# Optimization experiments

Hardware: AMD Instinct MI355X
Metric: run time of the kernel (lower is better)

The kernel has to match this reference:

```python
import jax, jax.numpy as jnp
import numpy as np

INPUT_DIM = 1024
HEAD_DIM = 64
BATCH = 4
SEQ = 2048


def setup_inputs() -> dict:
    key = jax.random.key(0)
    ks = jax.random.split(key, 7)
    scale = 1.0 / np.sqrt(INPUT_DIM)
    x = jax.random.normal(ks[0], (BATCH, SEQ, INPUT_DIM), dtype=jnp.float32)
    Wq = jax.random.uniform(ks[1], (INPUT_DIM, HEAD_DIM), jnp.float32, -scale, scale)
    bq = jax.random.uniform(ks[2], (HEAD_DIM,), jnp.float32, -scale, scale)
    Wk = jax.random.uniform(ks[3], (INPUT_DIM, HEAD_DIM), jnp.float32, -scale, scale)
    bk = jax.random.uniform(ks[4], (HEAD_DIM,), jnp.float32, -scale, scale)
    Wv = jax.random.uniform(ks[5], (INPUT_DIM, HEAD_DIM), jnp.float32, -scale, scale)
    bv = jax.random.uniform(ks[6], (HEAD_DIM,), jnp.float32, -scale, scale)
    return {"x": x, "Wq": Wq, "bq": bq, "Wk": Wk, "bk": bk, "Wv": Wv, "bv": bv}


def reference(x, Wq, bq, Wk, bk, Wv, bv):
    # q,k,v: [B, S, Hd]
    q = jnp.einsum('bsd,dh->bsh', x, Wq) + bq
    k = jnp.einsum('bsd,dh->bsh', x, Wk) + bk
    v = jnp.einsum('bsd,dh->bsh', x, Wv) + bv
    scores = jnp.einsum('bqh,bkh->bqk', q, k)  # [B, S, S]
    S = scores.shape[-1]
    # causal mask: 0 on/below diagonal, -inf above (matches torch triu().T trick)
    causal = jnp.tril(jnp.ones((S, S), dtype=bool))
    scores = jnp.where(causal, scores, -jnp.inf)
    # original divides by sqrt(head_dim) AFTER adding mask (-inf stays -inf)
    scores = scores / jnp.sqrt(jnp.asarray(q.shape[-1], scores.dtype))
    attn = jax.nn.softmax(scores, axis=-1)
    return jnp.einsum('bqk,bkh->bqh', attn, v)
```

## Files before the change

### kernel.cpp

```cpp
#include <hip/hip_runtime.h>

#define SEQ  2048
#define DIM  1024
#define HD   64
#define AW   4

typedef float f32x4  __attribute__((ext_vector_type(4)));
typedef short bf16x8 __attribute__((ext_vector_type(8)));

__device__ __forceinline__ short f2bf(float x) {
    union { float f; unsigned u; } v; v.f = x;
    unsigned r = v.u + 0x7FFFu + ((v.u >> 16) & 1u);
    return (short)(r >> 16);
}
__device__ __forceinline__ short f2bf_fast(float x) {
    union { float f; unsigned u; } v; v.f = x;
    return (short)((v.u + 0x8000u) >> 16);
}

#define MFMA16(a, b, c) __builtin_amdgcn_mfma_f32_16x16x32_bf16((a), (b), (c), 0, 0, 0)

__global__ __launch_bounds__(256) void wprep_kernel(
    const float* __restrict__ Wq, const float* __restrict__ Wk,
    const float* __restrict__ Wv, short* __restrict__ wfrag)
{
    const int idx = blockIdx.x * 256 + threadIdx.x;
    const int l  = idx & 63;
    const int n  = (idx >> 6) & 3;
    const int ks = (idx >> 8) & 31;
    const int w  = idx >> 13;
    const float* __restrict__ W = (w == 0) ? Wq : (w == 1) ? Wk : Wv;
    bf16x8 v;
#pragma unroll
    for (int j = 0; j < 8; ++j)
        v[j] = f2bf(W[(size_t)(ks * 32 + (l >> 4) * 8 + j) * HD + n * 16 + (l & 15)]);
    *reinterpret_cast<bf16x8*>(wfrag + (size_t)idx * 8) = v;
}

__global__ __launch_bounds__(256) void proj_kernel(
    const float* __restrict__ x, const short* __restrict__ wfrag,
    const float* __restrict__ bq, const float* __restrict__ bk,
    const float* __restrict__ bv,
    short* __restrict__ Qs, short* __restrict__ Kb, short* __restrict__ Vt)
{
    __shared__ __align__(16) char smem[49152 + 2304];

    const int tid  = threadIdx.x;
    const int lane = tid & 63;
    const int w    = tid >> 6;
    const int c    = lane & 15;
    const int g    = lane >> 4;
    const int r0   = blockIdx.x * 16;

    f32x4 acc[3][4] = {};
    for (int ks = w * 8; ks < w * 8 + 8; ++ks) {
        const float* xp = x + (size_t)(r0 + c) * DIM + ks * 32 + g * 8;
        float4 a0 = *reinterpret_cast<const float4*>(xp);
        float4 a1 = *reinterpret_cast<const float4*>(xp + 4);
        float av[8] = {a0.x, a0.y, a0.z, a0.w, a1.x, a1.y, a1.z, a1.w};
        bf16x8 af;
#pragma unroll
        for (int j = 0; j < 8; ++j) af[j] = f2bf_fast(av[j]);
#pragma unroll
        for (int which = 0; which < 3; ++which)
#pragma unroll
            for (int n = 0; n < 4; ++n) {
                bf16x8 bfr = *reinterpret_cast<const bf16x8*>(
                    wfrag + ((size_t)((which * 32 + ks) * 4 + n) * 64 + lane) * 8);
                acc[which][n] = MFMA16(af, bfr, acc[which][n]);
            }
    }

    f32x4* red = (f32x4*)smem;
#pragma unroll
    for (int which = 0; which < 3; ++which)
#pragma unroll
        for (int n = 0; n < 4; ++n)
            red[((which * 4 + n) * 4 + w) * 64 + lane] = acc[which][n];
    __syncthreads();

    if (w < 3) {
        const float* __restrict__ bias = (w == 0) ? bq : (w == 1) ? bk : bv;
        f32x4 sum[4];
#pragma unroll
        for (int n = 0; n < 4; ++n) {
            sum[n] = red[((w * 4 + n) * 4 + 0) * 64 + lane];
#pragma unroll
            for (int s = 1; s < 4; ++s)
                sum[n] += red[((w * 4 + n) * 4 + s) * 64 + lane];
        }
        if (w < 2) {
            short* __restrict__ o = (w == 0) ? Qs : Kb;
            const float sc = (w == 0) ? 0.125f : 1.0f;
#pragma unroll
            for (int n = 0; n < 4; ++n) {
                const float bb = bias[n * 16 + c];
#pragma unroll
                for (int i = 0; i < 4; ++i)
                    o[(size_t)(r0 + g * 4 + i) * HD + n * 16 + c] =
                        f2bf((sum[n][i] + bb) * sc);
            }
        } else {
            short* ts = (short*)(smem + 49152);
#pragma unroll
            for (int n = 0; n < 4; ++n) {
                const float bb = bias[n * 16 + c];
#pragma unroll
                for (int i = 0; i < 4; ++i)
                    ts[(g * 4 + i) * 72 + n * 16 + c] = f2bf(sum[n][i] + bb);
            }
            bf16x8 o0, o1;
#pragma unroll
            for (int e = 0; e < 8; ++e) o0[e] = ts[e * 72 + lane];
#pragma unroll
            for (int e = 0; e < 8; ++e) o1[e] = ts[(8 + e) * 72 + lane];
            const int b  = r0 >> 11;
            const int sb = r0 & (SEQ - 1);
            short* dst = Vt + (((size_t)(b * 64 + lane)) << 11) + sb;
            *reinterpret_cast<bf16x8*>(dst)     = o0;
            *reinterpret_cast<bf16x8*>(dst + 8) = o1;
        }
    }
}

__device__ __forceinline__ void loadK(
    const short* __restrict__ Kb, size_t krow0, int key0, int c, int g,
    bf16x8 (&kf)[4][2])
{
#pragma unroll
    for (int n = 0; n < 4; ++n)
#pragma unroll
        for (int st = 0; st < 2; ++st)
            kf[n][st] = *reinterpret_cast<const bf16x8*>(
                Kb + (krow0 + key0 + n * 16 + c) * HD + st * 32 + g * 8);
}

__device__ __forceinline__ void tile_step(
    const short* __restrict__ Vt, int batch, int t, int tlast, int qbase,
    int c, int g, short* P, bf16x8 qf0, bf16x8 qf1,
    const bf16x8 (&kf)[4][2],
    f32x4 (&O)[4], float (&m_i)[4], float (&l_i)[4])
{
    const int key0 = t * 64;

    bf16x8 vf[2][4];
#pragma unroll
    for (int st = 0; st < 2; ++st)
#pragma unroll
        for (int n = 0; n < 4; ++n)
            vf[st][n] = *reinterpret_cast<const bf16x8*>(
                Vt + (((size_t)(batch * 64 + n * 16 + c)) << 11) + key0 + st * 32 + g * 8);

    f32x4 S[4] = {};
#pragma unroll
    for (int n = 0; n < 4; ++n) {
        S[n] = MFMA16(qf0, kf[n][0], S[n]);
        S[n] = MFMA16(qf1, kf[n][1], S[n]);
    }
    if (t == tlast) {
#pragma unroll
        for (int n = 0; n < 4; ++n)
#pragma unroll
            for (int i = 0; i < 4; ++i)
                if (key0 + n * 16 + c > qbase + g * 4 + i)
                    S[n][i] = -__builtin_inff();
    }
    float mx[4], corr[4], rs[4];
#pragma unroll
    for (int i = 0; i < 4; ++i)
        mx[i] = fmaxf(fmaxf(S[0][i], S[1][i]), fmaxf(S[2][i], S[3][i]));
#pragma unroll
    for (int off = 1; off <= 8; off <<= 1)
#pragma unroll
        for (int i = 0; i < 4; ++i)
            mx[i] = fmaxf(mx[i], __shfl_xor(mx[i], off, 64));
#pragma unroll
    for (int i = 0; i < 4; ++i) {
        const float mn = fmaxf(m_i[i], mx[i]);
        corr[i] = __expf(m_i[i] - mn);
        m_i[i] = mn;
        rs[i] = 0.f;
    }
#pragma unroll
    for (int n = 0; n < 4; ++n)
#pragma unroll
        for (int i = 0; i < 4; ++i) {
            const float p = __expf(S[n][i] - m_i[i]);
            S[n][i] = p;
            rs[i] += p;
        }
#pragma unroll
    for (int off = 1; off <= 8; off <<= 1)
#pragma unroll
        for (int i = 0; i < 4; ++i)
            rs[i] += __shfl_xor(rs[i], off, 64);
#pragma unroll
    for (int i = 0; i < 4; ++i) l_i[i] = l_i[i] * corr[i] + rs[i];
#pragma unroll
    for (int n = 0; n < 4; ++n)
#pragma unroll
        for (int i = 0; i < 4; ++i) O[n][i] *= corr[i];
#pragma unroll
    for (int n = 0; n < 4; ++n)
#pragma unroll
        for (int i = 0; i < 4; ++i)
            P[(g * 4 + i) * 72 + n * 16 + c] = f2bf_fast(S[n][i]);
#pragma unroll
    for (int st = 0; st < 2; ++st) {
        bf16x8 pf = *reinterpret_cast<const bf16x8*>(&P[c * 72 + st * 32 + g * 8]);
#pragma unroll
        for (int n = 0; n < 4; ++n)
            O[n] = MFMA16(pf, vf[st][n], O[n]);
    }
}

__global__ __launch_bounds__(256) void attn_fused_kernel(
    const short* __restrict__ Qs, const short* __restrict__ Kb,
    const short* __restrict__ Vt, float* __restrict__ out)
{
    __shared__ float  Ost[AW][2][16][68];
    __shared__ float2 mlst[AW][2][16];
    __shared__ short  Pw[AW][16 * 72];

    const int tid  = threadIdx.x;
    const int lane = tid & 63;
    const int w    = tid >> 6;
    const int c    = lane & 15;
    const int g    = lane >> 4;

    const int batch = blockIdx.x >> 6;
    const int p     = blockIdx.x & 63;
    const int qlocA = p;
    const int qlocB = 127 - p;
    const int ntA   = (qlocA >> 2) + 1;
    const int ntB   = (qlocB >> 2) + 1;
    const int qbA   = batch * 128 + qlocA;
    const int qbB   = batch * 128 + qlocB;

    bf16x8 qfA0 = *reinterpret_cast<const bf16x8*>(Qs + (size_t)(qbA * 16 + c) * HD + g * 8);
    bf16x8 qfA1 = *reinterpret_cast<const bf16x8*>(Qs + (size_t)(qbA * 16 + c) * HD + 32 + g * 8);
    bf16x8 qfB0 = *reinterpret_cast<const bf16x8*>(Qs + (size_t)(qbB * 16 + c) * HD + g * 8);
    bf16x8 qfB1 = *reinterpret_cast<const bf16x8*>(Qs + (size_t)(qbB * 16 + c) * HD + 32 + g * 8);

    f32x4 OA[4] = {}, OB[4] = {};
    float mA[4], lA[4], mB[4], lB[4];
#pragma unroll
    for (int i = 0; i < 4; ++i) {
        mA[i] = -__builtin_inff(); lA[i] = 0.f;
        mB[i] = -__builtin_inff(); lB[i] = 0.f;
    }

    short* P = Pw[w];
    const size_t krow0 = (size_t)batch * SEQ;

    bf16x8 kf[4][2], kfn[4][2];
    if (w < 33) {
        const int t0 = (w < ntA) ? w : w - ntA;
        loadK(Kb, krow0, t0 * 64, c, g, kf);
    }
    for (int idx = w; idx < 33; idx += AW) {
        const int nidx = idx + AW;
        int tn;
        if (nidx < 33) tn = (nidx < ntA) ? nidx : nidx - ntA;
        else           tn = (idx  < ntA) ? idx  : idx  - ntA;
        loadK(Kb, krow0, tn * 64, c, g, kfn);

        if (idx < ntA)
            tile_step(Vt, batch, idx, ntA - 1, qlocA * 16,
                      c, g, P, qfA0, qfA1, kf, OA, mA, lA);
        else
            tile_step(Vt, batch, idx - ntA, ntB - 1, qlocB * 16,
                      c, g, P, qfB0, qfB1, kf, OB, mB, lB);

#pragma unroll
        for (int n = 0; n < 4; ++n) {
            kf[n][0] = kfn[n][0];
            kf[n][1] = kfn[n][1];
        }
    }

#pragma unroll
    for (int n = 0; n < 4; ++n)
#pragma unroll
        for (int i = 0; i < 4; ++i) {
            Ost[w][0][g * 4 + i][n * 16 + c] = OA[n][i];
            Ost[w][1][g * 4 + i][n * 16 + c] = OB[n][i];
        }
    if (c == 0) {
#pragma unroll
        for (int i = 0; i < 4; ++i) {
            mlst[w][0][g * 4 + i] = make_float2(mA[i], lA[i]);
            mlst[w][1][g * 4 + i] = make_float2(mB[i], lB[i]);
        }
    }
    __syncthreads();

    {
        const int s  = w >> 1;
        const int qb = (w >> 1) ? qbB : qbA;
#pragma unroll
        for (int ri = 0; ri < 8; ++ri) {
            const int row = (w & 1) * 8 + ri;
            float M = -__builtin_inff();
#pragma unroll
            for (int wv = 0; wv < AW; ++wv)
                M = fmaxf(M, mlst[wv][s][row].x);
            float l = 0.f, o = 0.f;
#pragma unroll
            for (int wv = 0; wv < AW; ++wv) {
                const float2 ml = mlst[wv][s][row];
                const float wgt = __expf(ml.x - M);
                l += wgt * ml.y;
                o += wgt * Ost[wv][s][row][lane];
            }
            out[(size_t)(qb * 16 + row) * HD + lane] = o / l;
        }
    }
}

extern "C" void kernel_launch(void* const* d_in, const int* in_sizes, int n_in,
                              void* d_out, int out_size, void* d_ws, size_t ws_size,
                              hipStream_t stream)
{
    (void)in_sizes; (void)n_in; (void)out_size; (void)ws_size;
    const float* x  = (const float*)d_in[0];
    const float* Wq = (const float*)d_in[1];
    const float* bq = (const float*)d_in[2];
    const float* Wk = (const float*)d_in[3];
    const float* bk = (const float*)d_in[4];
    const float* Wv = (const float*)d_in[5];
    const float* bv = (const float*)d_in[6];
    float* out = (float*)d_out;

    char* ws = (char*)d_ws;
    short* Qs    = (short*)(ws);
    short* Kb    = (short*)(ws + (1u << 20));
    short* Vt    = (short*)(ws + (2u << 20));
    short* wfrag = (short*)(ws + (3u << 20));

    wprep_kernel<<<96, 256, 0, stream>>>(Wq, Wk, Wv, wfrag);
    proj_kernel<<<512, 256, 0, stream>>>(x, wfrag, bq, bk, bv, Qs, Kb, Vt);
    attn_fused_kernel<<<256, 256, 0, stream>>>(Qs, Kb, Vt, out);
}
```

Measured before the change: 43.45 us.

## Share K/V tile loads across paired query blocks and use exp2 softmax

The attention loop is restructured so that for key tiles both paired query blocks need (t < ntA), each K and V tile is loaded once and used for both query blocks, with separate P buffers per block. The remaining tiles for the long query block run in a second loop that prefetches K. Softmax switches to exp2f, with log2(e) folded into the Q scale factor, so each exponential skips a multiply. The shared-tile loop drops the K register prefetch, which may expose more load latency, and it raises register pressure because two S accumulators are live at once.

```diff
diff --git a/kernel.cpp b/kernel.cpp
--- a/kernel.cpp
+++ b/kernel.cpp
@@ -19,6 +19,8 @@
 }
 
 #define MFMA16(a, b, c) __builtin_amdgcn_mfma_f32_16x16x32_bf16((a), (b), (c), 0, 0, 0)
+
+#define QSCALE 0.18033688011f
 
 __global__ __launch_bounds__(256) void wprep_kernel(
     const float* __restrict__ Wq, const float* __restrict__ Wk,
@@ -91,7 +93,7 @@
         }
         if (w < 2) {
             short* __restrict__ o = (w == 0) ? Qs : Kb;
-            const float sc = (w == 0) ? 0.125f : 1.0f;
+            const float sc = (w == 0) ? QSCALE : 1.0f;
 #pragma unroll
             for (int n = 0; n < 4; ++n) {
                 const float bb = bias[n * 16 + c];
@@ -134,30 +136,34 @@
             kf[n][st] = *reinterpret_cast<const bf16x8*>(
                 Kb + (krow0 + key0 + n * 16 + c) * HD + st * 32 + g * 8);
 }
-
-__device__ __forceinline__ void tile_step(
-    const short* __restrict__ Vt, int batch, int t, int tlast, int qbase,
-    int c, int g, short* P, bf16x8 qf0, bf16x8 qf1,
-    const bf16x8 (&kf)[4][2],
-    f32x4 (&O)[4], float (&m_i)[4], float (&l_i)[4])
-{
-    const int key0 = t * 64;
-
-    bf16x8 vf[2][4];
+__device__ __forceinline__ void loadV(
+    const short* __restrict__ Vt, int batch, int key0, int c, int g,
+    bf16x8 (&vf)[2][4])
+{
 #pragma unroll
     for (int st = 0; st < 2; ++st)
 #pragma unroll
         for (int n = 0; n < 4; ++n)
             vf[st][n] = *reinterpret_cast<const bf16x8*>(
                 Vt + (((size_t)(batch * 64 + n * 16 + c)) << 11) + key0 + st * 32 + g * 8);
-
-    f32x4 S[4] = {};
+}
+
+__device__ __forceinline__ void qk16(
+    const bf16x8 (&kf)[4][2], bf16x8 q0, bf16x8 q1, f32x4 (&S)[4])
+{
 #pragma unroll
     for (int n = 0; n < 4; ++n) {
-        S[n] = MFMA16(qf0, kf[n][0], S[n]);
-        S[n] = MFMA16(qf1, kf[n][1], S[n]);
-    }
-    if (t == tlast) {
+        S[n] = MFMA16(q0, kf[n][0], S[n]);
+        S[n] = MFMA16(q1, kf[n][1], S[n]);
+    }
+}
+
+__device__ __forceinline__ void smax_pv(
+    f32x4 (&S)[4], bool diag, int key0, int qbase, int c, int g,
+    short* P, const bf16x8 (&vf)[2][4],
+    f32x4 (&O)[4], float (&m_i)[4], float (&l_i)[4])
+{
+    if (diag) {
 #pragma unroll
         for (int n = 0; n < 4; ++n)
 #pragma unroll
@@ -177,7 +183,7 @@
 #pragma unroll
     for (int i = 0; i < 4; ++i) {
         const float mn = fmaxf(m_i[i], mx[i]);
-        corr[i] = __expf(m_i[i] - mn);
+        corr[i] = exp2f(m_i[i] - mn);
         m_i[i] = mn;
         rs[i] = 0.f;
     }
@@ -185,7 +191,7 @@
     for (int n = 0; n < 4; ++n)
 #pragma unroll
         for (int i = 0; i < 4; ++i) {
-            const float p = __expf(S[n][i] - m_i[i]);
+            const float p = exp2f(S[n][i] - m_i[i]);
             S[n][i] = p;
             rs[i] += p;
         }
@@ -220,7 +226,7 @@
 {
     __shared__ float  Ost[AW][2][16][68];
     __shared__ float2 mlst[AW][2][16];
-    __shared__ short  Pw[AW][16 * 72];
+    __shared__ short  Pw[AW][2][16 * 72];
 
     const int tid  = threadIdx.x;
     const int lane = tid & 63;
@@ -250,32 +256,39 @@
         mB[i] = -__builtin_inff(); lB[i] = 0.f;
     }
 
-    short* P = Pw[w];
+    short* PA = Pw[w][0];
+    short* PB = Pw[w][1];
     const size_t krow0 = (size_t)batch * SEQ;
 
-    bf16x8 kf[4][2], kfn[4][2];
-    if (w < 33) {
-        const int t0 = (w < ntA) ? w : w - ntA;
-        loadK(Kb, krow0, t0 * 64, c, g, kf);
-    }
-    for (int idx = w; idx < 33; idx += AW) {
-        const int nidx = idx + AW;
-        int tn;
-        if (nidx < 33) tn = (nidx < ntA) ? nidx : nidx - ntA;
-        else           tn = (idx  < ntA) ? idx  : idx  - ntA;
-        loadK(Kb, krow0, tn * 64, c, g, kfn);
-
-        if (idx < ntA)
-            tile_step(Vt, batch, idx, ntA - 1, qlocA * 16,
-                      c, g, P, qfA0, qfA1, kf, OA, mA, lA);
-        else
-            tile_step(Vt, batch, idx - ntA, ntB - 1, qlocB * 16,
-                      c, g, P, qfB0, qfB1, kf, OB, mB, lB);
-
-#pragma unroll
-        for (int n = 0; n < 4; ++n) {
-            kf[n][0] = kfn[n][0];
-            kf[n][1] = kfn[n][1];
+    for (int t = w; t < ntA; t += AW) {
+        bf16x8 kf[4][2];
+        bf16x8 vf[2][4];
+        loadK(Kb, krow0, t * 64, c, g, kf);
+        loadV(Vt, batch, t * 64, c, g, vf);
+        f32x4 SA[4] = {}, SB[4] = {};
+        qk16(kf, qfA0, qfA1, SA);
+        qk16(kf, qfB0, qfB1, SB);
+        smax_pv(SA, t == ntA - 1, t * 64, qlocA * 16, c, g, PA, vf, OA, mA, lA);
+        smax_pv(SB, false,        t * 64, qlocB * 16, c, g, PB, vf, OB, mB, lB);
+    }
+
+    {
+        int t2 = ntA + (((w - ntA) % AW) + AW) % AW;
+        bf16x8 kf[4][2], kfn[4][2];
+        if (t2 < ntB) loadK(Kb, krow0, t2 * 64, c, g, kf);
+        for (int t = t2; t < ntB; t += AW) {
+            const int tn = (t + AW < ntB) ? t + AW : t;
+            loadK(Kb, krow0, tn * 64, c, g, kfn);
+            bf16x8 vf[2][4];
+            loadV(Vt, batch, t * 64, c, g, vf);
+            f32x4 SB[4] = {};
+            qk16(kf, qfB0, qfB1, SB);
+            smax_pv(SB, t == ntB - 1, t * 64, qlocB * 16, c, g, PB, vf, OB, mB, lB);
+#pragma unroll
+            for (int n = 0; n < 4; ++n) {
+                kf[n][0] = kfn[n][0];
+                kf[n][1] = kfn[n][1];
+            }
         }
     }
 
@@ -309,7 +322,7 @@
 #pragma unroll
             for (int wv = 0; wv < AW; ++wv) {
                 const float2 ml = mlst[wv][s][row];
-                const float wgt = __expf(ml.x - M);
+                const float wgt = exp2f(ml.x - M);
                 l += wgt * ml.y;
                 o += wgt * Ost[wv][s][row][lane];
             }
```

Result: no change. 42.88 us (-1.3%).
